# Kernel tuning notes

Hardware: AMD Instinct MI355X
Metric: run time of the kernel (lower is better)

Reference implementation:

```python
import jax, jax.numpy as jnp
import numpy as np

EPS = 1e-5  # torch BatchNorm2d default eps


def _conv1x1(x, W, b):
    # x: [B,C,H,W], W: [O,C], b: [O]
    return jnp.einsum('bchw,oc->bohw', x, W) + b[None, :, None, None]


def _bn_eval(y, gamma, beta, mean, var):
    inv = gamma / jnp.sqrt(var + EPS)
    return y * inv[None, :, None, None] + (beta - mean * inv)[None, :, None, None]


def setup_inputs() -> dict:
    key = jax.random.key(0)
    ks = jax.random.split(key, 12)
    B, C, H, W = 4, 256, 64, 64
    mid = C // 4  # k = 4
    sc_in = (2.0 / C) ** 0.5   # kaiming_normal fan_in = C for 1x1 conv
    sc_mid = (2.0 / mid) ** 0.5
    x = jax.random.normal(ks[0], (B, C, H, W), jnp.float32)
    Wf = jax.random.normal(ks[1], (mid, C), jnp.float32) * sc_in
    bf = jnp.zeros((mid,), jnp.float32)
    gamma_f = jnp.ones((mid,), jnp.float32)
    beta_f = jnp.zeros((mid,), jnp.float32)
    mean_f = jax.random.normal(ks[2], (mid,), jnp.float32) * 0.1
    var_f = jax.random.uniform(ks[3], (mid,), jnp.float32, 0.5, 1.5)
    Wg = jax.random.normal(ks[4], (mid, C), jnp.float32) * sc_in
    bg = jnp.zeros((mid,), jnp.float32)
    gamma_g = jnp.ones((mid,), jnp.float32)
    beta_g = jnp.zeros((mid,), jnp.float32)
    mean_g = jax.random.normal(ks[5], (mid,), jnp.float32) * 0.1
    var_g = jax.random.uniform(ks[6], (mid,), jnp.float32, 0.5, 1.5)
    Wh = jax.random.normal(ks[7], (mid, C), jnp.float32) * sc_in
    bh = jnp.zeros((mid,), jnp.float32)
    # v conv is constant-initialized to 0 in the original; use small random
    # weights so the attention branch contributes to the output under test.
    Wv = jax.random.normal(ks[8], (C, mid), jnp.float32) * sc_mid * 0.1
    bv = jnp.zeros((C,), jnp.float32)
    v0 = jax.random.normal(ks[9], (B, H * W, 1), jnp.float32)  # power-iter init
    return dict(x=x, Wf=Wf, bf=bf, gamma_f=gamma_f, beta_f=beta_f, mean_f=mean_f,
                var_f=var_f, Wg=Wg, bg=bg, gamma_g=gamma_g, beta_g=beta_g,
                mean_g=mean_g, var_g=var_g, Wh=Wh, bh=bh, Wv=Wv, bv=bv, v0=v0)


def reference(x, Wf, bf, gamma_f, beta_f, mean_f, var_f,
              Wg, bg, gamma_g, beta_g, mean_g, var_g,
              Wh, bh, Wv, bv, v0):
    B, C, H, W = x.shape
    mid = Wf.shape[0]
    HW = H * W
    f_x = jax.nn.relu(_bn_eval(_conv1x1(x, Wf, bf), gamma_f, beta_f, mean_f, var_f)).reshape(B, mid, HW)
    g_x = jax.nn.relu(_bn_eval(_conv1x1(x, Wg, bg), gamma_g, beta_g, mean_g, var_g)).reshape(B, mid, HW)
    h_x = _conv1x1(x, Wh, bh).reshape(B, mid, HW)
    # dense non-local correlation: [B, HW, HW]
    z = jnp.einsum('bcn,bcm->bnm', f_x, g_x)
    # power iteration (Ip=1) for spectral-norm estimate
    v = jnp.einsum('bnm,bmk->bnk', z, v0)          # [B,HW,1]
    v = v / jnp.linalg.norm(v[:, :, 0], axis=1)[:, None, None]
    s = jnp.einsum('bn,bnm,bm->b', v[:, :, 0], z, v[:, :, 0])[:, None, None]
    attn = z / s
    z2 = jnp.einsum('bnm,bcm->bcn', attn, h_x).reshape(B, mid, H, W)
    return _conv1x1(z2, Wv, bv) + x
```

## Files before the change

### kernel.cpp

```cpp
#include <hip/hip_runtime.h>

#define NB   4
#define CIN  256
#define MID  64
#define HW   4096

typedef __attribute__((ext_vector_type(8))) short bfrag8;
typedef __attribute__((ext_vector_type(4))) float facc4;

constexpr size_t OFF_FGHT  = 0;
constexpr size_t OFF_FHI   = 8388608;
constexpr size_t OFF_FLO   = 10485760;
constexpr size_t OFF_WHI   = 12582912;
constexpr size_t OFF_WLO   = 12681216;
constexpr size_t OFF_BEFF  = 12779520;
constexpr size_t OFF_W2HI  = 12780544;
constexpr size_t OFF_W2LO  = 12911616;
constexpr size_t OFF_MPART = 13042688;
constexpr size_t OFF_T     = 17236992;
constexpr size_t OFF_FGVU  = 17238016;
constexpr size_t OFF_NSQ   = 17240064;

__device__ __forceinline__ unsigned short f2bf(float f) {
    union { float f; unsigned u; } v; v.f = f;
    unsigned r = v.u + 0x7FFF + ((v.u >> 16) & 1);
    return (unsigned short)(r >> 16);
}
__device__ __forceinline__ float bf2f(unsigned short h) {
    union { unsigned u; float f; } v; v.u = ((unsigned)h) << 16;
    return v.f;
}
__device__ __forceinline__ void split_bf(float v, unsigned short& hi, unsigned short& lo) {
    hi = f2bf(v);
    lo = f2bf(v - bf2f(hi));
}

__global__ void k_weff(const float* __restrict__ Wf, const float* __restrict__ bf,
                       const float* __restrict__ gf, const float* __restrict__ btf,
                       const float* __restrict__ mf, const float* __restrict__ vf,
                       const float* __restrict__ Wg, const float* __restrict__ bg,
                       const float* __restrict__ gg, const float* __restrict__ btg,
                       const float* __restrict__ mg, const float* __restrict__ vg,
                       const float* __restrict__ Wh, const float* __restrict__ bh,
                       unsigned short* __restrict__ whi, unsigned short* __restrict__ wlo,
                       float* __restrict__ beff) {
    const int o = blockIdx.x;
    const int c = threadIdx.x;
    float w, sh;
    if (o < 64) {
        float inv = gf[o] * rsqrtf(vf[o] + 1e-5f);
        w  = Wf[o * CIN + c] * inv;
        sh = bf[o] * inv + btf[o] - mf[o] * inv;
    } else if (o < 128) {
        int oo = o - 64;
        float inv = gg[oo] * rsqrtf(vg[oo] + 1e-5f);
        w  = Wg[oo * CIN + c] * inv;
        sh = bg[oo] * inv + btg[oo] - mg[oo] * inv;
    } else {
        int oo = o - 128;
        w  = Wh[oo * CIN + c];
        sh = bh[oo];
    }
    unsigned short hi, lo; split_bf(w, hi, lo);
    whi[o * CIN + c] = hi;
    wlo[o * CIN + c] = lo;
    if (c == 0) beff[o] = sh;
}

__launch_bounds__(512)
__global__ void k_fgh2(const float* __restrict__ x,
                       const unsigned short* __restrict__ whi_g,
                       const unsigned short* __restrict__ wlo_g,
                       const float* __restrict__ beff,
                       const float* __restrict__ v0,
                       float* __restrict__ fghT,
                       unsigned short* __restrict__ fhi,
                       unsigned short* __restrict__ flo,
                       float* __restrict__ tvec,
                       float* __restrict__ mpart) {
    __shared__ unsigned short xh[64][72], xl[64][72];
    __shared__ char wbuf[2 * 192 * 72 * 2];
    unsigned short (*wh)[72] = (unsigned short(*)[72])wbuf;
    unsigned short (*wl)[72] = (unsigned short(*)[72])(wbuf + 192 * 72 * 2);

    const int nb = blockIdx.x, b = blockIdx.y;
    const int n0 = nb * 64;
    const int tid = threadIdx.x, l = tid & 63, w = tid >> 6;
    const int wo = w >> 1, wn = w & 1;
    const int lr = l & 15, lk = l >> 4;
    facc4 acc[2][3];
    #pragma unroll
    for (int i = 0; i < 2; ++i)
        #pragma unroll
        for (int j = 0; j < 3; ++j) acc[i][j] = (facc4){0.f, 0.f, 0.f, 0.f};

    const int cr = tid >> 4, nq = tid & 15;

    for (int kc = 0; kc < 4; ++kc) {
        const int c0 = kc * 64;
        {
            const float* xr = x + ((size_t)(b * CIN + c0 + cr * 2)) * HW + n0 + nq * 4;
            float4 va = *(const float4*)xr;
            float4 vb = *(const float4*)(xr + HW);
            #pragma unroll
            for (int i = 0; i < 4; ++i) {
                float fa = (&va.x)[i], fb = (&vb.x)[i];
                unsigned short ha, la, hb, lb;
                split_bf(fa, ha, la);
                split_bf(fb, hb, lb);
                const int n = nq * 4 + i;
                *(unsigned int*)&xh[n][cr * 2] = (unsigned int)ha | ((unsigned int)hb << 16);
                *(unsigned int*)&xl[n][cr * 2] = (unsigned int)la | ((unsigned int)lb << 16);
            }
        }
        {
            #pragma unroll
            for (int k = 0; k < 3; ++k) {
                const int id = tid + k * 512;
                const int orow = id >> 3, cs = id & 7;
                *(bfrag8*)&wh[orow][cs * 8] = *(const bfrag8*)(whi_g + orow * CIN + c0 + cs * 8);
                *(bfrag8*)&wl[orow][cs * 8] = *(const bfrag8*)(wlo_g + orow * CIN + c0 + cs * 8);
            }
        }
        __syncthreads();
        #pragma unroll
        for (int ks = 0; ks < 2; ++ks) {
            bfrag8 ah[2], al[2];
            #pragma unroll
            for (int s = 0; s < 2; ++s) {
                ah[s] = *(const bfrag8*)&xh[wn * 32 + s * 16 + lr][ks * 32 + lk * 8];
                al[s] = *(const bfrag8*)&xl[wn * 32 + s * 16 + lr][ks * 32 + lk * 8];
            }
            #pragma unroll
            for (int so = 0; so < 3; ++so) {
                bfrag8 bh = *(const bfrag8*)&wh[wo * 48 + so * 16 + lr][ks * 32 + lk * 8];
                bfrag8 bl = *(const bfrag8*)&wl[wo * 48 + so * 16 + lr][ks * 32 + lk * 8];
                #pragma unroll
                for (int sn = 0; sn < 2; ++sn) {
                    acc[sn][so] = __builtin_amdgcn_mfma_f32_16x16x32_bf16(ah[sn], bh, acc[sn][so], 0, 0, 0);
                    acc[sn][so] = __builtin_amdgcn_mfma_f32_16x16x32_bf16(ah[sn], bl, acc[sn][so], 0, 0, 0);
                    acc[sn][so] = __builtin_amdgcn_mfma_f32_16x16x32_bf16(al[sn], bh, acc[sn][so], 0, 0, 0);
                }
            }
        }
        __syncthreads();
    }

    float (*mls)[136]  = (float(*)[136])wbuf;
    float (*tred)[64]  = (float(*)[64])(wbuf + 36864);
    float* v0ls        = (float*)xh;

    #pragma unroll
    for (int so = 0; so < 3; ++so) {
        const int o = wo * 48 + so * 16 + lr;
        const float bias = beff[o];
        const bool rl = (o < 128);
        #pragma unroll
        for (int sn = 0; sn < 2; ++sn)
            #pragma unroll
            for (int r = 0; r < 4; ++r) {
                const int nn = wn * 32 + sn * 16 + lk * 4 + r;
                const int n = n0 + nn;
                float v = acc[sn][so][r] + bias;
                if (rl) v = fmaxf(v, 0.0f);
                if (o < 128) fghT[((size_t)(b * HW) + n) * 128 + o] = v;
                if (o < 64) {
                    unsigned short hi, lo; split_bf(v, hi, lo);
                    fhi[((size_t)(b * HW) + n) * MID + o] = hi;
                    flo[((size_t)(b * HW) + n) * MID + o] = lo;
                }
                if (o >= 64) mls[nn][o - 64] = v;
            }
    }
    if (tid < 64) v0ls[tid] = v0[(size_t)b * HW + n0 + tid];
    __syncthreads();

    {
        const int c = tid & 63, ng = tid >> 6;
        float tp = 0.f;
        #pragma unroll
        for (int i = 0; i < 8; ++i) {
            const int nn = ng * 8 + i;
            tp = fmaf(mls[nn][c], v0ls[nn], tp);
        }
        tred[ng][c] = tp;
    }
    {
        const int tcp = tid >> 4, tc = tid & 15;
        const int cp = tcp * 2, cc = tc * 4;
        float macc[2][4];
        #pragma unroll
        for (int i = 0; i < 2; ++i)
            #pragma unroll
            for (int j = 0; j < 4; ++j) macc[i][j] = 0.f;
        for (int nn = 0; nn < 64; ++nn) {
            const float g0 = mls[nn][cp], g1 = mls[nn][cp + 1];
            const float h0 = mls[nn][64 + cc + 0], h1 = mls[nn][64 + cc + 1];
            const float h2 = mls[nn][64 + cc + 2], h3 = mls[nn][64 + cc + 3];
            macc[0][0] = fmaf(g0, h0, macc[0][0]); macc[0][1] = fmaf(g0, h1, macc[0][1]);
            macc[0][2] = fmaf(g0, h2, macc[0][2]); macc[0][3] = fmaf(g0, h3, macc[0][3]);
            macc[1][0] = fmaf(g1, h0, macc[1][0]); macc[1][1] = fmaf(g1, h1, macc[1][1]);
            macc[1][2] = fmaf(g1, h2, macc[1][2]); macc[1][3] = fmaf(g1, h3, macc[1][3]);
        }
        const size_t mpb = ((size_t)(b * 64 + nb) * 64) * 64;
        *(float4*)&mpart[mpb + (size_t)(cp + 0) * 64 + cc] =
            make_float4(macc[0][0], macc[0][1], macc[0][2], macc[0][3]);
        *(float4*)&mpart[mpb + (size_t)(cp + 1) * 64 + cc] =
            make_float4(macc[1][0], macc[1][1], macc[1][2], macc[1][3]);
    }
    __syncthreads();
    if (tid < 64) {
        float s = 0.f;
        #pragma unroll
        for (int g = 0; g < 8; ++g) s += tred[g][tid];
        atomicAdd(&tvec[b * MID + tid], s);
    }
}

__launch_bounds__(256)
__global__ void k_vfg(const float* __restrict__ fghT, const float* __restrict__ t,
                      float* __restrict__ fgvu, float* __restrict__ nsq) {
    __shared__ float ts[64];
    __shared__ float vuls[256];
    __shared__ float red2[8][128];
    __shared__ float rs[4];
    const int b = blockIdx.y, n0 = blockIdx.x * 256;
    const int tid = threadIdx.x;
    if (tid < 64) ts[tid] = t[b * MID + tid];
    __syncthreads();
    const int nl = tid >> 2, q = tid & 3;
    float mynsq = 0.f;
    for (int ps = 0; ps < 4; ++ps) {
        const int n = n0 + ps * 64 + nl;
        const float* p = fghT + ((size_t)(b * HW) + n) * 128 + q * 16;
        float a = 0.f;
        #pragma unroll
        for (int u = 0; u < 4; ++u) {
            float4 fv = *(const float4*)(p + u * 4);
            a = fmaf(fv.x, ts[q * 16 + u * 4 + 0], a);
            a = fmaf(fv.y, ts[q * 16 + u * 4 + 1], a);
            a = fmaf(fv.z, ts[q * 16 + u * 4 + 2], a);
            a = fmaf(fv.w, ts[q * 16 + u * 4 + 3], a);
        }
        a += __shfl_xor(a, 1);
        a += __shfl_xor(a, 2);
        if (q == 0) { vuls[ps * 64 + nl] = a; mynsq += a * a; }
    }
    {
        float s = mynsq;
        #pragma unroll
        for (int off = 32; off > 0; off >>= 1) s += __shfl_down(s, off);
        if ((tid & 63) == 0) rs[tid >> 6] = s;
        __syncthreads();
        if (tid == 0) atomicAdd(&nsq[b], rs[0] + rs[1] + rs[2] + rs[3]);
    }
    const int rq = tid & 31, ng2 = tid >> 5;
    float a2[4] = {0.f, 0.f, 0.f, 0.f};
    for (int it = 0; it < 32; ++it) {
        const int ni = ng2 + 8 * it;
        float4 fv = *(const float4*)(fghT + ((size_t)(b * HW) + n0 + ni) * 128 + rq * 4);
        const float vv = vuls[ni];
        a2[0] = fmaf(fv.x, vv, a2[0]); a2[1] = fmaf(fv.y, vv, a2[1]);
        a2[2] = fmaf(fv.z, vv, a2[2]); a2[3] = fmaf(fv.w, vv, a2[3]);
    }
    #pragma unroll
    for (int i = 0; i < 4; ++i) red2[ng2][rq * 4 + i] = a2[i];
    __syncthreads();
    if (tid < 128) {
        float s = 0.f;
        #pragma unroll
        for (int g = 0; g < 8; ++g) s += red2[g][tid];
        atomicAdd(&fgvu[b * 128 + tid], s);
    }
}

__launch_bounds__(256)
__global__ void k_w2s(const float* __restrict__ Wv, const float* __restrict__ mpart,
                      const float* __restrict__ fgvu, const float* __restrict__ nsq,
                      unsigned short* __restrict__ w2hi, unsigned short* __restrict__ w2lo) {
    __shared__ float Mc[8][64];
    __shared__ float svs;
    const int cp0 = blockIdx.x * 8, b = blockIdx.y;
    const int tid = threadIdx.x;
    {
        const int c = tid & 63;
        const int r0 = tid >> 6, r1 = r0 + 4;
        float s0 = 0.f, s1 = 0.f;
        for (int nb = 0; nb < 64; ++nb) {
            const size_t base = ((size_t)(b * 64 + nb) * 64) * 64;
            s0 += mpart[base + (size_t)(cp0 + r0) * 64 + c];
            s1 += mpart[base + (size_t)(cp0 + r1) * 64 + c];
        }
        Mc[r0][c] = s0;
        Mc[r1][c] = s1;
    }
    if (tid < 64) {
        float a = fgvu[b * 128 + tid] * fgvu[b * 128 + 64 + tid];
        #pragma unroll
        for (int off = 32; off > 0; off >>= 1) a += __shfl_down(a, off);
        if (tid == 0) svs = a / nsq[b];
    }
    __syncthreads();
    const float inv_s = 1.0f / svs;
    const int o = tid;
    float wv[64];
    #pragma unroll
    for (int u = 0; u < 16; ++u) {
        float4 w4 = *(const float4*)(Wv + o * MID + u * 4);
        wv[u * 4 + 0] = w4.x; wv[u * 4 + 1] = w4.y; wv[u * 4 + 2] = w4.z; wv[u * 4 + 3] = w4.w;
    }
    unsigned short rh[8] __attribute__((aligned(16)));
    unsigned short rl[8] __attribute__((aligned(16)));
    #pragma unroll
    for (int j = 0; j < 8; ++j) {
        float a = 0.f;
        #pragma unroll
        for (int c = 0; c < 64; ++c) a = fmaf(wv[c], Mc[j][c], a);
        split_bf(a * inv_s, rh[j], rl[j]);
    }
    const size_t base = ((size_t)(b * CIN) + o) * MID + cp0;
    *(bfrag8*)(w2hi + base) = *(const bfrag8*)rh;
    *(bfrag8*)(w2lo + base) = *(const bfrag8*)rl;
}

__launch_bounds__(256)
__global__ void k_out(const float* __restrict__ x,
                      const unsigned short* __restrict__ fhi, const unsigned short* __restrict__ flo,
                      const unsigned short* __restrict__ w2hi, const unsigned short* __restrict__ w2lo,
                      const float* __restrict__ bv, float* __restrict__ out) {
    __shared__ unsigned short fh[64][72], fl[64][72], wh[64][72], wl[64][72];
    const int n0 = blockIdx.x * 64;
    const int o0 = blockIdx.y * 64;
    const int b  = blockIdx.z;
    const int tid = threadIdx.x, l = tid & 63, w = tid >> 6;
    const int wo = w >> 1, wn = w & 1;
    const int lr = l & 15, lk = l >> 4;
    #pragma unroll
    for (int i = 0; i < 2; ++i) {
        int ch = tid + i * 256;
        int row = ch >> 3, cs = ch & 7;
        const size_t fsrc = ((size_t)(b * HW) + n0 + row) * MID + cs * 8;
        const size_t wsrc = ((size_t)(b * CIN) + o0 + row) * MID + cs * 8;
        *(bfrag8*)&fh[row][cs * 8] = *(const bfrag8*)(fhi + fsrc);
        *(bfrag8*)&fl[row][cs * 8] = *(const bfrag8*)(flo + fsrc);
        *(bfrag8*)&wh[row][cs * 8] = *(const bfrag8*)(w2hi + wsrc);
        *(bfrag8*)&wl[row][cs * 8] = *(const bfrag8*)(w2lo + wsrc);
    }
    __syncthreads();
    facc4 acc[2][2];
    #pragma unroll
    for (int i = 0; i < 2; ++i)
        #pragma unroll
        for (int j = 0; j < 2; ++j) acc[i][j] = (facc4){0.f, 0.f, 0.f, 0.f};
    #pragma unroll
    for (int ks = 0; ks < 2; ++ks) {
        bfrag8 ah[2], al[2], bh[2], bl[2];
        #pragma unroll
        for (int s = 0; s < 2; ++s) {
            ah[s] = *(const bfrag8*)&wh[wo * 32 + s * 16 + lr][ks * 32 + lk * 8];
            al[s] = *(const bfrag8*)&wl[wo * 32 + s * 16 + lr][ks * 32 + lk * 8];
            bh[s] = *(const bfrag8*)&fh[wn * 32 + s * 16 + lr][ks * 32 + lk * 8];
            bl[s] = *(const bfrag8*)&fl[wn * 32 + s * 16 + lr][ks * 32 + lk * 8];
        }
        #pragma unroll
        for (int so = 0; so < 2; ++so)
            #pragma unroll
            for (int sn = 0; sn < 2; ++sn) {
                acc[so][sn] = __builtin_amdgcn_mfma_f32_16x16x32_bf16(ah[so], bh[sn], acc[so][sn], 0, 0, 0);
                acc[so][sn] = __builtin_amdgcn_mfma_f32_16x16x32_bf16(ah[so], bl[sn], acc[so][sn], 0, 0, 0);
                acc[so][sn] = __builtin_amdgcn_mfma_f32_16x16x32_bf16(al[so], bh[sn], acc[so][sn], 0, 0, 0);
            }
    }
    #pragma unroll
    for (int so = 0; so < 2; ++so)
        #pragma unroll
        for (int r = 0; r < 4; ++r) {
            const int o = o0 + wo * 32 + so * 16 + lk * 4 + r;
            const float bias = bv[o];
            #pragma unroll
            for (int sn = 0; sn < 2; ++sn) {
                const int n = n0 + wn * 32 + sn * 16 + lr;
                const size_t idx = ((size_t)(b * CIN) + o) * HW + n;
                out[idx] = x[idx] + bias + acc[so][sn][r];
            }
        }
}

extern "C" void kernel_launch(void* const* d_in, const int* in_sizes, int n_in,
                              void* d_out, int out_size, void* d_ws, size_t ws_size,
                              hipStream_t stream) {
    const float* x   = (const float*)d_in[0];
    const float* Wf  = (const float*)d_in[1];
    const float* bf  = (const float*)d_in[2];
    const float* gaf = (const float*)d_in[3];
    const float* bef = (const float*)d_in[4];
    const float* mef = (const float*)d_in[5];
    const float* vaf = (const float*)d_in[6];
    const float* Wg  = (const float*)d_in[7];
    const float* bg  = (const float*)d_in[8];
    const float* gag = (const float*)d_in[9];
    const float* beg = (const float*)d_in[10];
    const float* meg = (const float*)d_in[11];
    const float* vag = (const float*)d_in[12];
    const float* Wh  = (const float*)d_in[13];
    const float* bh  = (const float*)d_in[14];
    const float* Wv  = (const float*)d_in[15];
    const float* bv  = (const float*)d_in[16];
    const float* v0  = (const float*)d_in[17];
    float* out = (float*)d_out;
    char* ws = (char*)d_ws;

    float*          fghT = (float*)(ws + OFF_FGHT);
    unsigned short* fhi  = (unsigned short*)(ws + OFF_FHI);
    unsigned short* flo  = (unsigned short*)(ws + OFF_FLO);
    unsigned short* whi  = (unsigned short*)(ws + OFF_WHI);
    unsigned short* wlo  = (unsigned short*)(ws + OFF_WLO);
    float*          beff = (float*)(ws + OFF_BEFF);
    unsigned short* w2hi = (unsigned short*)(ws + OFF_W2HI);
    unsigned short* w2lo = (unsigned short*)(ws + OFF_W2LO);
    float*          mpart= (float*)(ws + OFF_MPART);
    float*          tvec = (float*)(ws + OFF_T);
    float*          fgvu = (float*)(ws + OFF_FGVU);
    float*          nsq  = (float*)(ws + OFF_NSQ);

    hipMemsetAsync(tvec, 0, 3328, stream);

    k_weff<<<192, CIN, 0, stream>>>(Wf, bf, gaf, bef, mef, vaf,
                                    Wg, bg, gag, beg, meg, vag,
                                    Wh, bh, whi, wlo, beff);
    k_fgh2<<<dim3(HW / 64, NB), 512, 0, stream>>>(x, whi, wlo, beff, v0,
                                                  fghT, fhi, flo, tvec, mpart);
    k_vfg <<<dim3(16, NB), 256, 0, stream>>>(fghT, tvec, fgvu, nsq);
    k_w2s <<<dim3(8, NB), 256, 0, stream>>>(Wv, mpart, fgvu, nsq, w2hi, w2lo);
    k_out <<<dim3(HW / 64, CIN / 64, NB), 256, 0, stream>>>(x, fhi, flo, w2hi, w2lo, bv, out);
}
```

Before: 138.3 us.

## Fuse weight prep into projection kernel, halve tile, replace atomics with partials

Folds the BN weight-folding kernel into the projection kernel, which now reads the fp32 weights, scales them and splits them into bf16 hi/lo in shared memory on every block. The token tile drops from 64 to 32, giving twice as many blocks, and the memset plus atomicAdd reductions become per-block partial buffers reduced by the downstream kernels. The aim is to remove two launches and the atomic contention and to improve occupancy. The cost is redundant weight conversion in every block, twice the mpart partials for k_w2s to sum, and lower MFMA reuse per block.

```diff
diff --git a/kernel.cpp b/kernel.cpp
--- a/kernel.cpp
+++ b/kernel.cpp
@@ -4,6 +4,7 @@
 #define CIN  256
 #define MID  64
 #define HW   4096
+#define NBLK 128
 
 typedef __attribute__((ext_vector_type(8))) short bfrag8;
 typedef __attribute__((ext_vector_type(4))) float facc4;
@@ -11,15 +12,12 @@
 constexpr size_t OFF_FGHT  = 0;
 constexpr size_t OFF_FHI   = 8388608;
 constexpr size_t OFF_FLO   = 10485760;
-constexpr size_t OFF_WHI   = 12582912;
-constexpr size_t OFF_WLO   = 12681216;
-constexpr size_t OFF_BEFF  = 12779520;
-constexpr size_t OFF_W2HI  = 12780544;
-constexpr size_t OFF_W2LO  = 12911616;
-constexpr size_t OFF_MPART = 13042688;
-constexpr size_t OFF_T     = 17236992;
-constexpr size_t OFF_FGVU  = 17238016;
-constexpr size_t OFF_NSQ   = 17240064;
+constexpr size_t OFF_W2HI  = 12582912;
+constexpr size_t OFF_W2LO  = 12713984;
+constexpr size_t OFF_MPART = 12845056;
+constexpr size_t OFF_TPART = 21233664;
+constexpr size_t OFF_FGVUP = 21364736;
+constexpr size_t OFF_NSQP  = 21397504;
 
 __device__ __forceinline__ unsigned short f2bf(float f) {
     union { float f; unsigned u; } v; v.f = f;
@@ -35,82 +33,56 @@
     lo = f2bf(v - bf2f(hi));
 }
 
-__global__ void k_weff(const float* __restrict__ Wf, const float* __restrict__ bf,
-                       const float* __restrict__ gf, const float* __restrict__ btf,
-                       const float* __restrict__ mf, const float* __restrict__ vf,
-                       const float* __restrict__ Wg, const float* __restrict__ bg,
-                       const float* __restrict__ gg, const float* __restrict__ btg,
-                       const float* __restrict__ mg, const float* __restrict__ vg,
-                       const float* __restrict__ Wh, const float* __restrict__ bh,
-                       unsigned short* __restrict__ whi, unsigned short* __restrict__ wlo,
-                       float* __restrict__ beff) {
-    const int o = blockIdx.x;
-    const int c = threadIdx.x;
-    float w, sh;
-    if (o < 64) {
-        float inv = gf[o] * rsqrtf(vf[o] + 1e-5f);
-        w  = Wf[o * CIN + c] * inv;
-        sh = bf[o] * inv + btf[o] - mf[o] * inv;
-    } else if (o < 128) {
-        int oo = o - 64;
-        float inv = gg[oo] * rsqrtf(vg[oo] + 1e-5f);
-        w  = Wg[oo * CIN + c] * inv;
-        sh = bg[oo] * inv + btg[oo] - mg[oo] * inv;
-    } else {
-        int oo = o - 128;
-        w  = Wh[oo * CIN + c];
-        sh = bh[oo];
-    }
-    unsigned short hi, lo; split_bf(w, hi, lo);
-    whi[o * CIN + c] = hi;
-    wlo[o * CIN + c] = lo;
-    if (c == 0) beff[o] = sh;
-}
-
 __launch_bounds__(512)
 __global__ void k_fgh2(const float* __restrict__ x,
-                       const unsigned short* __restrict__ whi_g,
-                       const unsigned short* __restrict__ wlo_g,
-                       const float* __restrict__ beff,
+                       const float* __restrict__ Wf, const float* __restrict__ bf,
+                       const float* __restrict__ gaf, const float* __restrict__ btf,
+                       const float* __restrict__ mef, const float* __restrict__ vaf,
+                       const float* __restrict__ Wg, const float* __restrict__ bg,
+                       const float* __restrict__ gag, const float* __restrict__ btg,
+                       const float* __restrict__ meg, const float* __restrict__ vag,
+                       const float* __restrict__ Wh, const float* __restrict__ bh,
                        const float* __restrict__ v0,
                        float* __restrict__ fghT,
-                       unsigned short* __restrict__ fhi,
-                       unsigned short* __restrict__ flo,
-                       float* __restrict__ tvec,
-                       float* __restrict__ mpart) {
-    __shared__ unsigned short xh[64][72], xl[64][72];
-    __shared__ char wbuf[2 * 192 * 72 * 2];
+                       unsigned short* __restrict__ fhi, unsigned short* __restrict__ flo,
+                       float* __restrict__ tpart, float* __restrict__ mpart) {
+    __shared__ float invs[192], beffs[192];
+    __shared__ unsigned short xh[32][72], xl[32][72];
+    __shared__ char wbuf[55296];
     unsigned short (*wh)[72] = (unsigned short(*)[72])wbuf;
     unsigned short (*wl)[72] = (unsigned short(*)[72])(wbuf + 192 * 72 * 2);
 
     const int nb = blockIdx.x, b = blockIdx.y;
-    const int n0 = nb * 64;
+    const int n0 = nb * 32;
     const int tid = threadIdx.x, l = tid & 63, w = tid >> 6;
     const int wo = w >> 1, wn = w & 1;
     const int lr = l & 15, lk = l >> 4;
-    facc4 acc[2][3];
-    #pragma unroll
-    for (int i = 0; i < 2; ++i)
-        #pragma unroll
-        for (int j = 0; j < 3; ++j) acc[i][j] = (facc4){0.f, 0.f, 0.f, 0.f};
-
-    const int cr = tid >> 4, nq = tid & 15;
+
+    if (tid < 192) {
+        float inv, sh;
+        if (tid < 64)       { inv = gaf[tid] * rsqrtf(vaf[tid] + 1e-5f);
+                              sh = bf[tid] * inv + btf[tid] - mef[tid] * inv; }
+        else if (tid < 128) { int o = tid - 64; inv = gag[o] * rsqrtf(vag[o] + 1e-5f);
+                              sh = bg[o] * inv + btg[o] - meg[o] * inv; }
+        else                { inv = 1.0f; sh = bh[tid - 128]; }
+        invs[tid] = inv; beffs[tid] = sh;
+    }
+    __syncthreads();
+
+    facc4 acc[3];
+    #pragma unroll
+    for (int j = 0; j < 3; ++j) acc[j] = (facc4){0.f, 0.f, 0.f, 0.f};
 
     for (int kc = 0; kc < 4; ++kc) {
         const int c0 = kc * 64;
         {
-            const float* xr = x + ((size_t)(b * CIN + c0 + cr * 2)) * HW + n0 + nq * 4;
-            float4 va = *(const float4*)xr;
-            float4 vb = *(const float4*)(xr + HW);
+            const int c = tid >> 3, n4 = (tid & 7) * 4;
+            const float* xr = x + ((size_t)(b * CIN + c0 + c)) * HW + n0 + n4;
+            float4 v = *(const float4*)xr;
             #pragma unroll
             for (int i = 0; i < 4; ++i) {
-                float fa = (&va.x)[i], fb = (&vb.x)[i];
-                unsigned short ha, la, hb, lb;
-                split_bf(fa, ha, la);
-                split_bf(fb, hb, lb);
-                const int n = nq * 4 + i;
-                *(unsigned int*)&xh[n][cr * 2] = (unsigned int)ha | ((unsigned int)hb << 16);
-                *(unsigned int*)&xl[n][cr * 2] = (unsigned int)la | ((unsigned int)lb << 16);
+                unsigned short hi, lo; split_bf((&v.x)[i], hi, lo);
+                xh[n4 + i][c] = hi; xl[n4 + i][c] = lo;
             }
         }
         {
@@ -118,72 +90,83 @@
             for (int k = 0; k < 3; ++k) {
                 const int id = tid + k * 512;
                 const int orow = id >> 3, cs = id & 7;
-                *(bfrag8*)&wh[orow][cs * 8] = *(const bfrag8*)(whi_g + orow * CIN + c0 + cs * 8);
-                *(bfrag8*)&wl[orow][cs * 8] = *(const bfrag8*)(wlo_g + orow * CIN + c0 + cs * 8);
+                const float* wrow;
+                if (orow < 64)       wrow = Wf + orow * CIN;
+                else if (orow < 128) wrow = Wg + (orow - 64) * CIN;
+                else                 wrow = Wh + (orow - 128) * CIN;
+                const float inv = invs[orow];
+                float4 a4 = *(const float4*)(wrow + c0 + cs * 8);
+                float4 b4 = *(const float4*)(wrow + c0 + cs * 8 + 4);
+                unsigned short h8[8] __attribute__((aligned(16)));
+                unsigned short l8[8] __attribute__((aligned(16)));
+                #pragma unroll
+                for (int i = 0; i < 4; ++i) split_bf((&a4.x)[i] * inv, h8[i], l8[i]);
+                #pragma unroll
+                for (int i = 0; i < 4; ++i) split_bf((&b4.x)[i] * inv, h8[4 + i], l8[4 + i]);
+                *(bfrag8*)&wh[orow][cs * 8] = *(const bfrag8*)h8;
+                *(bfrag8*)&wl[orow][cs * 8] = *(const bfrag8*)l8;
             }
         }
         __syncthreads();
         #pragma unroll
         for (int ks = 0; ks < 2; ++ks) {
-            bfrag8 ah[2], al[2];
-            #pragma unroll
-            for (int s = 0; s < 2; ++s) {
-                ah[s] = *(const bfrag8*)&xh[wn * 32 + s * 16 + lr][ks * 32 + lk * 8];
-                al[s] = *(const bfrag8*)&xl[wn * 32 + s * 16 + lr][ks * 32 + lk * 8];
-            }
+            bfrag8 ah = *(const bfrag8*)&xh[wn * 16 + lr][ks * 32 + lk * 8];
+            bfrag8 al = *(const bfrag8*)&xl[wn * 16 + lr][ks * 32 + lk * 8];
             #pragma unroll
             for (int so = 0; so < 3; ++so) {
-                bfrag8 bh = *(const bfrag8*)&wh[wo * 48 + so * 16 + lr][ks * 32 + lk * 8];
-                bfrag8 bl = *(const bfrag8*)&wl[wo * 48 + so * 16 + lr][ks * 32 + lk * 8];
-                #pragma unroll
-                for (int sn = 0; sn < 2; ++sn) {
-                    acc[sn][so] = __builtin_amdgcn_mfma_f32_16x16x32_bf16(ah[sn], bh, acc[sn][so], 0, 0, 0);
-                    acc[sn][so] = __builtin_amdgcn_mfma_f32_16x16x32_bf16(ah[sn], bl, acc[sn][so], 0, 0, 0);
-                    acc[sn][so] = __builtin_amdgcn_mfma_f32_16x16x32_bf16(al[sn], bh, acc[sn][so], 0, 0, 0);
-                }
+                bfrag8 bh8 = *(const bfrag8*)&wh[wo * 48 + so * 16 + lr][ks * 32 + lk * 8];
+                bfrag8 bl8 = *(const bfrag8*)&wl[wo * 48 + so * 16 + lr][ks * 32 + lk * 8];
+                acc[so] = __builtin_amdgcn_mfma_f32_16x16x32_bf16(ah, bh8, acc[so], 0, 0, 0);
+                acc[so] = __builtin_amdgcn_mfma_f32_16x16x32_bf16(ah, bl8, acc[so], 0, 0, 0);
+                acc[so] = __builtin_amdgcn_mfma_f32_16x16x32_bf16(al, bh8, acc[so], 0, 0, 0);
             }
         }
         __syncthreads();
     }
 
-    float (*mls)[136]  = (float(*)[136])wbuf;
-    float (*tred)[64]  = (float(*)[64])(wbuf + 36864);
-    float* v0ls        = (float*)xh;
+    float (*mls)[136] = (float(*)[136])wbuf;
+    float (*tred)[64] = (float(*)[64])(wbuf + 17408);
+    float* v0ls       = (float*)(wbuf + 17408 + 2048);
 
     #pragma unroll
     for (int so = 0; so < 3; ++so) {
         const int o = wo * 48 + so * 16 + lr;
-        const float bias = beff[o];
+        const float bias = beffs[o];
         const bool rl = (o < 128);
         #pragma unroll
-        for (int sn = 0; sn < 2; ++sn)
-            #pragma unroll
-            for (int r = 0; r < 4; ++r) {
-                const int nn = wn * 32 + sn * 16 + lk * 4 + r;
-                const int n = n0 + nn;
-                float v = acc[sn][so][r] + bias;
-                if (rl) v = fmaxf(v, 0.0f);
-                if (o < 128) fghT[((size_t)(b * HW) + n) * 128 + o] = v;
-                if (o < 64) {
-                    unsigned short hi, lo; split_bf(v, hi, lo);
-                    fhi[((size_t)(b * HW) + n) * MID + o] = hi;
-                    flo[((size_t)(b * HW) + n) * MID + o] = lo;
-                }
-                if (o >= 64) mls[nn][o - 64] = v;
-            }
-    }
-    if (tid < 64) v0ls[tid] = v0[(size_t)b * HW + n0 + tid];
+        for (int r = 0; r < 4; ++r) {
+            const int nn = wn * 16 + lk * 4 + r;
+            const int n = n0 + nn;
+            float v = acc[so][r] + bias;
+            if (rl) v = fmaxf(v, 0.0f);
+            if (o < 128) fghT[((size_t)(b * HW) + n) * 128 + o] = v;
+            if (o < 64) {
+                unsigned short hi, lo; split_bf(v, hi, lo);
+                fhi[((size_t)(b * HW) + n) * MID + o] = hi;
+                flo[((size_t)(b * HW) + n) * MID + o] = lo;
+            }
+            if (o >= 64) mls[nn][o - 64] = v;
+        }
+    }
+    if (tid < 32) v0ls[tid] = v0[(size_t)b * HW + n0 + tid];
     __syncthreads();
 
     {
         const int c = tid & 63, ng = tid >> 6;
         float tp = 0.f;
         #pragma unroll
-        for (int i = 0; i < 8; ++i) {
-            const int nn = ng * 8 + i;
+        for (int i = 0; i < 4; ++i) {
+            const int nn = ng * 4 + i;
             tp = fmaf(mls[nn][c], v0ls[nn], tp);
         }
         tred[ng][c] = tp;
+    }
+    __syncthreads();
+    if (tid < 64) {
+        float s = 0.f;
+        #pragma unroll
+        for (int g = 0; g < 8; ++g) s += tred[g][tid];
+        tpart[((size_t)(b * NBLK) + nb) * 64 + tid] = s;
     }
     {
         const int tcp = tid >> 4, tc = tid & 15;
@@ -193,7 +176,7 @@
         for (int i = 0; i < 2; ++i)
             #pragma unroll
             for (int j = 0; j < 4; ++j) macc[i][j] = 0.f;
-        for (int nn = 0; nn < 64; ++nn) {
+        for (int nn = 0; nn < 32; ++nn) {
             const float g0 = mls[nn][cp], g1 = mls[nn][cp + 1];
             const float h0 = mls[nn][64 + cc + 0], h1 = mls[nn][64 + cc + 1];
             const float h2 = mls[nn][64 + cc + 2], h3 = mls[nn][64 + cc + 3];
@@ -202,31 +185,34 @@
             macc[1][0] = fmaf(g1, h0, macc[1][0]); macc[1][1] = fmaf(g1, h1, macc[1][1]);
             macc[1][2] = fmaf(g1, h2, macc[1][2]); macc[1][3] = fmaf(g1, h3, macc[1][3]);
         }
-        const size_t mpb = ((size_t)(b * 64 + nb) * 64) * 64;
+        const size_t mpb = ((size_t)(b * NBLK) + nb) * 4096;
         *(float4*)&mpart[mpb + (size_t)(cp + 0) * 64 + cc] =
             make_float4(macc[0][0], macc[0][1], macc[0][2], macc[0][3]);
         *(float4*)&mpart[mpb + (size_t)(cp + 1) * 64 + cc] =
             make_float4(macc[1][0], macc[1][1], macc[1][2], macc[1][3]);
     }
-    __syncthreads();
-    if (tid < 64) {
-        float s = 0.f;
-        #pragma unroll
-        for (int g = 0; g < 8; ++g) s += tred[g][tid];
-        atomicAdd(&tvec[b * MID + tid], s);
-    }
 }
 
 __launch_bounds__(256)
-__global__ void k_vfg(const float* __restrict__ fghT, const float* __restrict__ t,
-                      float* __restrict__ fgvu, float* __restrict__ nsq) {
+__global__ void k_vfg(const float* __restrict__ fghT, const float* __restrict__ tpart,
+                      float* __restrict__ fgvu_part, float* __restrict__ nsq_part) {
+    __shared__ float tred4[4][64];
     __shared__ float ts[64];
     __shared__ float vuls[256];
     __shared__ float red2[8][128];
     __shared__ float rs[4];
-    const int b = blockIdx.y, n0 = blockIdx.x * 256;
+    const int chunk = blockIdx.x, b = blockIdx.y, n0 = chunk * 256;
     const int tid = threadIdx.x;
-    if (tid < 64) ts[tid] = t[b * MID + tid];
+    {
+        const int c = tid & 63, grp = tid >> 6;
+        float s = 0.f;
+        #pragma unroll 8
+        for (int i = 0; i < 32; ++i)
+            s += tpart[((size_t)(b * NBLK) + grp * 32 + i) * 64 + c];
+        tred4[grp][c] = s;
+    }
+    __syncthreads();
+    if (tid < 64) ts[tid] = tred4[0][tid] + tred4[1][tid] + tred4[2][tid] + tred4[3][tid];
     __syncthreads();
     const int nl = tid >> 2, q = tid & 3;
     float mynsq = 0.f;
@@ -252,7 +238,7 @@
         for (int off = 32; off > 0; off >>= 1) s += __shfl_down(s, off);
         if ((tid & 63) == 0) rs[tid >> 6] = s;
         __syncthreads();
-        if (tid == 0) atomicAdd(&nsq[b], rs[0] + rs[1] + rs[2] + rs[3]);
+        if (tid == 0) nsq_part[b * 16 + chunk] = rs[0] + rs[1] + rs[2] + rs[3];
     }
     const int rq = tid & 31, ng2 = tid >> 5;
     float a2[4] = {0.f, 0.f, 0.f, 0.f};
@@ -270,13 +256,13 @@
         float s = 0.f;
         #pragma unroll
         for (int g = 0; g < 8; ++g) s += red2[g][tid];
-        atomicAdd(&fgvu[b * 128 + tid], s);
+        fgvu_part[(size_t)(b * 16 + chunk) * 128 + tid] = s;
     }
 }
 
 __launch_bounds__(256)
 __global__ void k_w2s(const float* __restrict__ Wv, const float* __restrict__ mpart,
-                      const float* __restrict__ fgvu, const float* __restrict__ nsq,
+                      const float* __restrict__ fgvu_part, const float* __restrict__ nsq_part,
                       unsigned short* __restrict__ w2hi, unsigned short* __restrict__ w2lo) {
     __shared__ float Mc[8][64];
     __shared__ float svs;
@@ -286,8 +272,8 @@
         const int c = tid & 63;
         const int r0 = tid >> 6, r1 = r0 + 4;
         float s0 = 0.f, s1 = 0.f;
-        for (int nb = 0; nb < 64; ++nb) {
-            const size_t base = ((size_t)(b * 64 + nb) * 64) * 64;
+        for (int nb = 0; nb < NBLK; ++nb) {
+            const size_t base = ((size_t)(b * NBLK) + nb) * 4096;
             s0 += mpart[base + (size_t)(cp0 + r0) * 64 + c];
             s1 += mpart[base + (size_t)(cp0 + r1) * 64 + c];
         }
@@ -295,10 +281,20 @@
         Mc[r1][c] = s1;
     }
     if (tid < 64) {
-        float a = fgvu[b * 128 + tid] * fgvu[b * 128 + 64 + tid];
-        #pragma unroll
-        for (int off = 32; off > 0; off >>= 1) a += __shfl_down(a, off);
-        if (tid == 0) svs = a / nsq[b];
+        float fv = 0.f, gv = 0.f, ns = 0.f;
+        #pragma unroll
+        for (int ch = 0; ch < 16; ++ch) {
+            fv += fgvu_part[(size_t)(b * 16 + ch) * 128 + tid];
+            gv += fgvu_part[(size_t)(b * 16 + ch) * 128 + 64 + tid];
+        }
+        if (tid < 16) ns = nsq_part[b * 16 + tid];
+        float a = fv * gv;
+        #pragma unroll
+        for (int off = 32; off > 0; off >>= 1) {
+            a += __shfl_down(a, off);
+            ns += __shfl_down(ns, off);
+        }
+        if (tid == 0) svs = a / ns;
     }
     __syncthreads();
     const float inv_s = 1.0f / svs;
@@ -413,24 +409,17 @@
     float*          fghT = (float*)(ws + OFF_FGHT);
     unsigned short* fhi  = (unsigned short*)(ws + OFF_FHI);
     unsigned short* flo  = (unsigned short*)(ws + OFF_FLO);
-    unsigned short* whi  = (unsigned short*)(ws + OFF_WHI);
-    unsigned short* wlo  = (unsigned short*)(ws + OFF_WLO);
-    float*          beff = (float*)(ws + OFF_BEFF);
     unsigned short* w2hi = (unsigned short*)(ws + OFF_W2HI);
     unsigned short* w2lo = (unsigned short*)(ws + OFF_W2LO);
     float*          mpart= (float*)(ws + OFF_MPART);
-    float*          tvec = (float*)(ws + OFF_T);
-    float*          fgvu = (float*)(ws + OFF_FGVU);
-    float*          nsq  = (float*)(ws + OFF_NSQ);
-
-    hipMemsetAsync(tvec, 0, 3328, stream);
-
-    k_weff<<<192, CIN, 0, stream>>>(Wf, bf, gaf, bef, mef, vaf,
-                                    Wg, bg, gag, beg, meg, vag,
-                                    Wh, bh, whi, wlo, beff);
-    k_fgh2<<<dim3(HW / 64, NB), 512, 0, stream>>>(x, whi, wlo, beff, v0,
-                                                  fghT, fhi, flo, tvec, mpart);
-    k_vfg <<<dim3(16, NB), 256, 0, stream>>>(fghT, tvec, fgvu, nsq);
-    k_w2s <<<dim3(8, NB), 256, 0, stream>>>(Wv, mpart, fgvu, nsq, w2hi, w2lo);
+    float*          tpart= (float*)(ws + OFF_TPART);
+    float*          fgvup= (float*)(ws + OFF_FGVUP);
+    float*          nsqp = (float*)(ws + OFF_NSQP);
+
+    k_fgh2<<<dim3(NBLK, NB), 512, 0, stream>>>(x, Wf, bf, gaf, bef, mef, vaf,
+                                               Wg, bg, gag, beg, meg, vag, Wh, bh,
+                                               v0, fghT, fhi, flo, tpart, mpart);
+    k_vfg <<<dim3(16, NB), 256, 0, stream>>>(fghT, tpart, fgvup, nsqp);
+    k_w2s <<<dim3(8, NB), 256, 0, stream>>>(Wv, mpart, fgvup, nsqp, w2hi, w2lo);
     k_out <<<dim3(HW / 64, CIN / 64, NB), 256, 0, stream>>>(x, fhi, flo, w2hi, w2lo, bv, out);
 }
```

New measurement: 146.1 us. 1.06x slower.

## Replace per-pixel power-iteration pass with small Gram-matrix algebra and deterministic reductions

Applied to the files above, without the earlier changes.

The fghT buffer and the k_vfg pass that re-read it are removed. The power-iteration numerator and denominator are now computed from 64x64 Gram matrices (F^T F, G^T F) accumulated per tile alongside G^T H, plus a t vector. The fgh tile shrinks to 32 pixels, which doubles the grid. Atomics and the memset are replaced by per-block partial buffers and a dedicated reduction kernel. In exchange, the partial-sum buffer grows and the reduction kernel must read a much larger mpart array.

```diff
diff --git a/kernel.cpp b/kernel.cpp
--- a/kernel.cpp
+++ b/kernel.cpp
@@ -4,22 +4,22 @@
 #define CIN  256
 #define MID  64
 #define HW   4096
+#define NBLK 128
 
 typedef __attribute__((ext_vector_type(8))) short bfrag8;
 typedef __attribute__((ext_vector_type(4))) float facc4;
 
-constexpr size_t OFF_FGHT  = 0;
-constexpr size_t OFF_FHI   = 8388608;
-constexpr size_t OFF_FLO   = 10485760;
-constexpr size_t OFF_WHI   = 12582912;
-constexpr size_t OFF_WLO   = 12681216;
-constexpr size_t OFF_BEFF  = 12779520;
-constexpr size_t OFF_W2HI  = 12780544;
-constexpr size_t OFF_W2LO  = 12911616;
-constexpr size_t OFF_MPART = 13042688;
-constexpr size_t OFF_T     = 17236992;
-constexpr size_t OFF_FGVU  = 17238016;
-constexpr size_t OFF_NSQ   = 17240064;
+constexpr size_t OFF_FHI   = 0;
+constexpr size_t OFF_FLO   = 2097152;
+constexpr size_t OFF_WHI   = 4194304;
+constexpr size_t OFF_WLO   = 4292608;
+constexpr size_t OFF_BEFF  = 4390912;
+constexpr size_t OFF_W2HI  = 4391936;
+constexpr size_t OFF_W2LO  = 4523008;
+constexpr size_t OFF_MPART = 4654080;
+constexpr size_t OFF_TPART = 29819904;
+constexpr size_t OFF_MFIN  = 29950976;
+constexpr size_t OFF_TFIN  = 30147584;
 
 __device__ __forceinline__ unsigned short f2bf(float f) {
     union { float f; unsigned u; } v; v.f = f;
@@ -73,44 +73,38 @@
                        const unsigned short* __restrict__ wlo_g,
                        const float* __restrict__ beff,
                        const float* __restrict__ v0,
-                       float* __restrict__ fghT,
-                       unsigned short* __restrict__ fhi,
-                       unsigned short* __restrict__ flo,
-                       float* __restrict__ tvec,
-                       float* __restrict__ mpart) {
-    __shared__ unsigned short xh[64][72], xl[64][72];
-    __shared__ char wbuf[2 * 192 * 72 * 2];
+                       unsigned short* __restrict__ fhi, unsigned short* __restrict__ flo,
+                       float* __restrict__ tpart, float* __restrict__ mpart) {
+    __shared__ float beffs[192];
+    __shared__ float v0ls[32];
+    __shared__ unsigned short xh[32][72], xl[32][72];
+    __shared__ char wbuf[55296];
     unsigned short (*wh)[72] = (unsigned short(*)[72])wbuf;
     unsigned short (*wl)[72] = (unsigned short(*)[72])(wbuf + 192 * 72 * 2);
 
     const int nb = blockIdx.x, b = blockIdx.y;
-    const int n0 = nb * 64;
+    const int n0 = nb * 32;
     const int tid = threadIdx.x, l = tid & 63, w = tid >> 6;
     const int wo = w >> 1, wn = w & 1;
     const int lr = l & 15, lk = l >> 4;
-    facc4 acc[2][3];
-    #pragma unroll
-    for (int i = 0; i < 2; ++i)
-        #pragma unroll
-        for (int j = 0; j < 3; ++j) acc[i][j] = (facc4){0.f, 0.f, 0.f, 0.f};
-
-    const int cr = tid >> 4, nq = tid & 15;
+
+    if (tid < 192) beffs[tid] = beff[tid];
+    if (tid < 32)  v0ls[tid] = v0[(size_t)b * HW + n0 + tid];
+
+    facc4 acc[3];
+    #pragma unroll
+    for (int j = 0; j < 3; ++j) acc[j] = (facc4){0.f, 0.f, 0.f, 0.f};
 
     for (int kc = 0; kc < 4; ++kc) {
         const int c0 = kc * 64;
         {
-            const float* xr = x + ((size_t)(b * CIN + c0 + cr * 2)) * HW + n0 + nq * 4;
-            float4 va = *(const float4*)xr;
-            float4 vb = *(const float4*)(xr + HW);
+            const int c = tid >> 3, n4 = (tid & 7) * 4;
+            const float* xr = x + ((size_t)(b * CIN + c0 + c)) * HW + n0 + n4;
+            float4 v = *(const float4*)xr;
             #pragma unroll
             for (int i = 0; i < 4; ++i) {
-                float fa = (&va.x)[i], fb = (&vb.x)[i];
-                unsigned short ha, la, hb, lb;
-                split_bf(fa, ha, la);
-                split_bf(fb, hb, lb);
-                const int n = nq * 4 + i;
-                *(unsigned int*)&xh[n][cr * 2] = (unsigned int)ha | ((unsigned int)hb << 16);
-                *(unsigned int*)&xl[n][cr * 2] = (unsigned int)la | ((unsigned int)lb << 16);
+                unsigned short hi, lo; split_bf((&v.x)[i], hi, lo);
+                xh[n4 + i][c] = hi; xl[n4 + i][c] = lo;
             }
         }
         {
@@ -125,180 +119,157 @@
         __syncthreads();
         #pragma unroll
         for (int ks = 0; ks < 2; ++ks) {
-            bfrag8 ah[2], al[2];
-            #pragma unroll
-            for (int s = 0; s < 2; ++s) {
-                ah[s] = *(const bfrag8*)&xh[wn * 32 + s * 16 + lr][ks * 32 + lk * 8];
-                al[s] = *(const bfrag8*)&xl[wn * 32 + s * 16 + lr][ks * 32 + lk * 8];
-            }
+            bfrag8 ah = *(const bfrag8*)&xh[wn * 16 + lr][ks * 32 + lk * 8];
+            bfrag8 al = *(const bfrag8*)&xl[wn * 16 + lr][ks * 32 + lk * 8];
             #pragma unroll
             for (int so = 0; so < 3; ++so) {
-                bfrag8 bh = *(const bfrag8*)&wh[wo * 48 + so * 16 + lr][ks * 32 + lk * 8];
-                bfrag8 bl = *(const bfrag8*)&wl[wo * 48 + so * 16 + lr][ks * 32 + lk * 8];
-                #pragma unroll
-                for (int sn = 0; sn < 2; ++sn) {
-                    acc[sn][so] = __builtin_amdgcn_mfma_f32_16x16x32_bf16(ah[sn], bh, acc[sn][so], 0, 0, 0);
-                    acc[sn][so] = __builtin_amdgcn_mfma_f32_16x16x32_bf16(ah[sn], bl, acc[sn][so], 0, 0, 0);
-                    acc[sn][so] = __builtin_amdgcn_mfma_f32_16x16x32_bf16(al[sn], bh, acc[sn][so], 0, 0, 0);
-                }
+                bfrag8 bh8 = *(const bfrag8*)&wh[wo * 48 + so * 16 + lr][ks * 32 + lk * 8];
+                bfrag8 bl8 = *(const bfrag8*)&wl[wo * 48 + so * 16 + lr][ks * 32 + lk * 8];
+                acc[so] = __builtin_amdgcn_mfma_f32_16x16x32_bf16(ah, bh8, acc[so], 0, 0, 0);
+                acc[so] = __builtin_amdgcn_mfma_f32_16x16x32_bf16(ah, bl8, acc[so], 0, 0, 0);
+                acc[so] = __builtin_amdgcn_mfma_f32_16x16x32_bf16(al, bh8, acc[so], 0, 0, 0);
             }
         }
         __syncthreads();
     }
 
-    float (*mls)[136]  = (float(*)[136])wbuf;
-    float (*tred)[64]  = (float(*)[64])(wbuf + 36864);
-    float* v0ls        = (float*)xh;
+    float (*mls)[200] = (float(*)[200])wbuf;
+    float (*tred)[64] = (float(*)[64])(wbuf + 25600);
 
     #pragma unroll
     for (int so = 0; so < 3; ++so) {
         const int o = wo * 48 + so * 16 + lr;
-        const float bias = beff[o];
+        const float bias = beffs[o];
         const bool rl = (o < 128);
         #pragma unroll
-        for (int sn = 0; sn < 2; ++sn)
-            #pragma unroll
-            for (int r = 0; r < 4; ++r) {
-                const int nn = wn * 32 + sn * 16 + lk * 4 + r;
-                const int n = n0 + nn;
-                float v = acc[sn][so][r] + bias;
-                if (rl) v = fmaxf(v, 0.0f);
-                if (o < 128) fghT[((size_t)(b * HW) + n) * 128 + o] = v;
-                if (o < 64) {
-                    unsigned short hi, lo; split_bf(v, hi, lo);
-                    fhi[((size_t)(b * HW) + n) * MID + o] = hi;
-                    flo[((size_t)(b * HW) + n) * MID + o] = lo;
-                }
-                if (o >= 64) mls[nn][o - 64] = v;
-            }
-    }
-    if (tid < 64) v0ls[tid] = v0[(size_t)b * HW + n0 + tid];
+        for (int r = 0; r < 4; ++r) {
+            const int nn = wn * 16 + lk * 4 + r;
+            float v = acc[so][r] + bias;
+            if (rl) v = fmaxf(v, 0.0f);
+            mls[nn][o] = v;
+            if (o < 64) {
+                unsigned short hi, lo; split_bf(v, hi, lo);
+                fhi[((size_t)(b * HW) + n0 + nn) * MID + o] = hi;
+                flo[((size_t)(b * HW) + n0 + nn) * MID + o] = lo;
+            }
+        }
+    }
     __syncthreads();
 
     {
         const int c = tid & 63, ng = tid >> 6;
         float tp = 0.f;
         #pragma unroll
-        for (int i = 0; i < 8; ++i) {
-            const int nn = ng * 8 + i;
-            tp = fmaf(mls[nn][c], v0ls[nn], tp);
+        for (int i = 0; i < 4; ++i) {
+            const int nn = ng * 4 + i;
+            tp = fmaf(mls[nn][64 + c], v0ls[nn], tp);
         }
         tred[ng][c] = tp;
     }
     {
         const int tcp = tid >> 4, tc = tid & 15;
         const int cp = tcp * 2, cc = tc * 4;
-        float macc[2][4];
+        float mM[2][4], mF[2][4], mG[2][4];
         #pragma unroll
         for (int i = 0; i < 2; ++i)
             #pragma unroll
-            for (int j = 0; j < 4; ++j) macc[i][j] = 0.f;
-        for (int nn = 0; nn < 64; ++nn) {
-            const float g0 = mls[nn][cp], g1 = mls[nn][cp + 1];
-            const float h0 = mls[nn][64 + cc + 0], h1 = mls[nn][64 + cc + 1];
-            const float h2 = mls[nn][64 + cc + 2], h3 = mls[nn][64 + cc + 3];
-            macc[0][0] = fmaf(g0, h0, macc[0][0]); macc[0][1] = fmaf(g0, h1, macc[0][1]);
-            macc[0][2] = fmaf(g0, h2, macc[0][2]); macc[0][3] = fmaf(g0, h3, macc[0][3]);
-            macc[1][0] = fmaf(g1, h0, macc[1][0]); macc[1][1] = fmaf(g1, h1, macc[1][1]);
-            macc[1][2] = fmaf(g1, h2, macc[1][2]); macc[1][3] = fmaf(g1, h3, macc[1][3]);
-        }
-        const size_t mpb = ((size_t)(b * 64 + nb) * 64) * 64;
-        *(float4*)&mpart[mpb + (size_t)(cp + 0) * 64 + cc] =
-            make_float4(macc[0][0], macc[0][1], macc[0][2], macc[0][3]);
-        *(float4*)&mpart[mpb + (size_t)(cp + 1) * 64 + cc] =
-            make_float4(macc[1][0], macc[1][1], macc[1][2], macc[1][3]);
+            for (int j = 0; j < 4; ++j) { mM[i][j] = 0.f; mF[i][j] = 0.f; mG[i][j] = 0.f; }
+        for (int nn = 0; nn < 32; ++nn) {
+            const float f0 = mls[nn][cp], f1 = mls[nn][cp + 1];
+            const float g0 = mls[nn][64 + cp], g1 = mls[nn][64 + cp + 1];
+            float4 fc = *(const float4*)&mls[nn][cc];
+            float4 hc = *(const float4*)&mls[nn][128 + cc];
+            #pragma unroll
+            for (int j = 0; j < 4; ++j) {
+                const float fcj = (&fc.x)[j], hcj = (&hc.x)[j];
+                mM[0][j] = fmaf(g0, hcj, mM[0][j]);  mM[1][j] = fmaf(g1, hcj, mM[1][j]);
+                mF[0][j] = fmaf(f0, fcj, mF[0][j]);  mF[1][j] = fmaf(f1, fcj, mF[1][j]);
+                mG[0][j] = fmaf(g0, fcj, mG[0][j]);  mG[1][j] = fmaf(g1, fcj, mG[1][j]);
+            }
+        }
+        const size_t base = ((size_t)(b * NBLK) + nb) * (192 * 64);
+        #pragma unroll
+        for (int i = 0; i < 2; ++i) {
+            *(float4*)&mpart[base + (size_t)(0   + cp + i) * 64 + cc] = make_float4(mM[i][0], mM[i][1], mM[i][2], mM[i][3]);
+            *(float4*)&mpart[base + (size_t)(64  + cp + i) * 64 + cc] = make_float4(mF[i][0], mF[i][1], mF[i][2], mF[i][3]);
+            *(float4*)&mpart[base + (size_t)(128 + cp + i) * 64 + cc] = make_float4(mG[i][0], mG[i][1], mG[i][2], mG[i][3]);
+        }
     }
     __syncthreads();
     if (tid < 64) {
         float s = 0.f;
         #pragma unroll
         for (int g = 0; g < 8; ++g) s += tred[g][tid];
-        atomicAdd(&tvec[b * MID + tid], s);
+        tpart[((size_t)(b * NBLK) + nb) * 64 + tid] = s;
     }
 }
 
 __launch_bounds__(256)
-__global__ void k_vfg(const float* __restrict__ fghT, const float* __restrict__ t,
-                      float* __restrict__ fgvu, float* __restrict__ nsq) {
-    __shared__ float ts[64];
-    __shared__ float vuls[256];
-    __shared__ float red2[8][128];
-    __shared__ float rs[4];
-    const int b = blockIdx.y, n0 = blockIdx.x * 256;
+__global__ void k_red(const float* __restrict__ mpart, const float* __restrict__ tpart,
+                      float* __restrict__ Mfin, float* __restrict__ tfin) {
+    __shared__ float tred2[4][64];
+    const int rb = blockIdx.x, b = blockIdx.y;
     const int tid = threadIdx.x;
-    if (tid < 64) ts[tid] = t[b * MID + tid];
-    __syncthreads();
-    const int nl = tid >> 2, q = tid & 3;
-    float mynsq = 0.f;
-    for (int ps = 0; ps < 4; ++ps) {
-        const int n = n0 + ps * 64 + nl;
-        const float* p = fghT + ((size_t)(b * HW) + n) * 128 + q * 16;
-        float a = 0.f;
-        #pragma unroll
-        for (int u = 0; u < 4; ++u) {
-            float4 fv = *(const float4*)(p + u * 4);
-            a = fmaf(fv.x, ts[q * 16 + u * 4 + 0], a);
-            a = fmaf(fv.y, ts[q * 16 + u * 4 + 1], a);
-            a = fmaf(fv.z, ts[q * 16 + u * 4 + 2], a);
-            a = fmaf(fv.w, ts[q * 16 + u * 4 + 3], a);
-        }
-        a += __shfl_xor(a, 1);
-        a += __shfl_xor(a, 2);
-        if (q == 0) { vuls[ps * 64 + nl] = a; mynsq += a * a; }
-    }
-    {
-        float s = mynsq;
-        #pragma unroll
-        for (int off = 32; off > 0; off >>= 1) s += __shfl_down(s, off);
-        if ((tid & 63) == 0) rs[tid >> 6] = s;
+    const int c = tid & 63, rq = tid >> 6;
+    #pragma unroll
+    for (int p = 0; p < 2; ++p) {
+        const int rr = rb * 8 + p * 4 + rq;
+        float s = 0.f;
+        for (int nb = 0; nb < NBLK; ++nb)
+            s += mpart[((size_t)(b * NBLK) + nb) * (192 * 64) + (size_t)rr * 64 + c];
+        Mfin[((size_t)(b * 192) + rr) * 64 + c] = s;
+    }
+    if (rb == 0) {
+        float s = 0.f;
+        #pragma unroll 8
+        for (int i = 0; i < 32; ++i)
+            s += tpart[((size_t)(b * NBLK) + rq * 32 + i) * 64 + c];
+        tred2[rq][c] = s;
         __syncthreads();
-        if (tid == 0) atomicAdd(&nsq[b], rs[0] + rs[1] + rs[2] + rs[3]);
-    }
-    const int rq = tid & 31, ng2 = tid >> 5;
-    float a2[4] = {0.f, 0.f, 0.f, 0.f};
-    for (int it = 0; it < 32; ++it) {
-        const int ni = ng2 + 8 * it;
-        float4 fv = *(const float4*)(fghT + ((size_t)(b * HW) + n0 + ni) * 128 + rq * 4);
-        const float vv = vuls[ni];
-        a2[0] = fmaf(fv.x, vv, a2[0]); a2[1] = fmaf(fv.y, vv, a2[1]);
-        a2[2] = fmaf(fv.z, vv, a2[2]); a2[3] = fmaf(fv.w, vv, a2[3]);
-    }
-    #pragma unroll
-    for (int i = 0; i < 4; ++i) red2[ng2][rq * 4 + i] = a2[i];
-    __syncthreads();
-    if (tid < 128) {
-        float s = 0.f;
-        #pragma unroll
-        for (int g = 0; g < 8; ++g) s += red2[g][tid];
-        atomicAdd(&fgvu[b * 128 + tid], s);
+        if (tid < 64) tfin[b * 64 + tid] = tred2[0][tid] + tred2[1][tid] + tred2[2][tid] + tred2[3][tid];
     }
 }
 
 __launch_bounds__(256)
-__global__ void k_w2s(const float* __restrict__ Wv, const float* __restrict__ mpart,
-                      const float* __restrict__ fgvu, const float* __restrict__ nsq,
+__global__ void k_w2s(const float* __restrict__ Wv, const float* __restrict__ Mfin,
+                      const float* __restrict__ tfin,
                       unsigned short* __restrict__ w2hi, unsigned short* __restrict__ w2lo) {
+    __shared__ float ts[64], uu[64], ww[64];
     __shared__ float Mc[8][64];
     __shared__ float svs;
     const int cp0 = blockIdx.x * 8, b = blockIdx.y;
     const int tid = threadIdx.x;
+    if (tid < 64) ts[tid] = tfin[b * 64 + tid];
     {
-        const int c = tid & 63;
-        const int r0 = tid >> 6, r1 = r0 + 4;
-        float s0 = 0.f, s1 = 0.f;
-        for (int nb = 0; nb < 64; ++nb) {
-            const size_t base = ((size_t)(b * 64 + nb) * 64) * 64;
-            s0 += mpart[base + (size_t)(cp0 + r0) * 64 + c];
-            s1 += mpart[base + (size_t)(cp0 + r1) * 64 + c];
-        }
-        Mc[r0][c] = s0;
-        Mc[r1][c] = s1;
-    }
+        const int e0 = tid, e1 = tid + 256;
+        Mc[e0 >> 6][e0 & 63] = Mfin[((size_t)(b * 192) + cp0 + (e0 >> 6)) * 64 + (e0 & 63)];
+        Mc[e1 >> 6][e1 & 63] = Mfin[((size_t)(b * 192) + cp0 + (e1 >> 6)) * 64 + (e1 & 63)];
+    }
+    __syncthreads();
+    if (tid < 128) {
+        const int i = tid & 63;
+        const float* row = Mfin + ((size_t)(b * 192) + (tid < 64 ? 64 : 128) + i) * 64;
+        float a = 0.f;
+        #pragma unroll
+        for (int u = 0; u < 16; ++u) {
+            float4 r4 = *(const float4*)(row + u * 4);
+            a = fmaf(r4.x, ts[u * 4 + 0], a);
+            a = fmaf(r4.y, ts[u * 4 + 1], a);
+            a = fmaf(r4.z, ts[u * 4 + 2], a);
+            a = fmaf(r4.w, ts[u * 4 + 3], a);
+        }
+        if (tid < 64) uu[i] = a; else ww[i] = a;
+    }
+    __syncthreads();
     if (tid < 64) {
-        float a = fgvu[b * 128 + tid] * fgvu[b * 128 + 64 + tid];
-        #pragma unroll
-        for (int off = 32; off > 0; off >>= 1) a += __shfl_down(a, off);
-        if (tid == 0) svs = a / nsq[b];
+        float num = uu[tid] * ww[tid];
+        float den = ts[tid] * uu[tid];
+        #pragma unroll
+        for (int off = 32; off > 0; off >>= 1) {
+            num += __shfl_down(num, off);
+            den += __shfl_down(den, off);
+        }
+        if (tid == 0) svs = num / den;
     }
     __syncthreads();
     const float inv_s = 1.0f / svs;
@@ -410,7 +381,6 @@
     float* out = (float*)d_out;
     char* ws = (char*)d_ws;
 
-    float*          fghT = (float*)(ws + OFF_FGHT);
     unsigned short* fhi  = (unsigned short*)(ws + OFF_FHI);
     unsigned short* flo  = (unsigned short*)(ws + OFF_FLO);
     unsigned short* whi  = (unsigned short*)(ws + OFF_WHI);
@@ -419,18 +389,16 @@
     unsigned short* w2hi = (unsigned short*)(ws + OFF_W2HI);
     unsigned short* w2lo = (unsigned short*)(ws + OFF_W2LO);
     float*          mpart= (float*)(ws + OFF_MPART);
-    float*          tvec = (float*)(ws + OFF_T);
-    float*          fgvu = (float*)(ws + OFF_FGVU);
-    float*          nsq  = (float*)(ws + OFF_NSQ);
-
-    hipMemsetAsync(tvec, 0, 3328, stream);
+    float*          tpart= (float*)(ws + OFF_TPART);
+    float*          Mfin = (float*)(ws + OFF_MFIN);
+    float*          tfin = (float*)(ws + OFF_TFIN);
 
     k_weff<<<192, CIN, 0, stream>>>(Wf, bf, gaf, bef, mef, vaf,
                                     Wg, bg, gag, beg, meg, vag,
                                     Wh, bh, whi, wlo, beff);
-    k_fgh2<<<dim3(HW / 64, NB), 512, 0, stream>>>(x, whi, wlo, beff, v0,
-                                                  fghT, fhi, flo, tvec, mpart);
-    k_vfg <<<dim3(16, NB), 256, 0, stream>>>(fghT, tvec, fgvu, nsq);
-    k_w2s <<<dim3(8, NB), 256, 0, stream>>>(Wv, mpart, fgvu, nsq, w2hi, w2lo);
+    k_fgh2<<<dim3(NBLK, NB), 512, 0, stream>>>(x, whi, wlo, beff, v0,
+                                               fhi, flo, tpart, mpart);
+    k_red <<<dim3(24, NB), 256, 0, stream>>>(mpart, tpart, Mfin, tfin);
+    k_w2s <<<dim3(8, NB), 256, 0, stream>>>(Wv, Mfin, tfin, w2hi, w2lo);
     k_out <<<dim3(HW / 64, CIN / 64, NB), 256, 0, stream>>>(x, fhi, flo, w2hi, w2lo, bv, out);
 }
```

Measured after the change: 154.2 us. 1.12x slower.
